# Optimization experiments

Hardware: AMD Instinct MI355X
Metric: run time of the kernel (lower is better)

The kernel has to match this reference:

```python
import jax, jax.numpy as jnp
import numpy as np

N_QUBITS = 8
N_LAYERS = 3
BATCH = 8192


def setup_inputs() -> dict:
    key = jax.random.key(0)
    k0, k1, k2, k3 = jax.random.split(key, 4)
    return {
        "x": jax.random.normal(k0, (BATCH, N_QUBITS), jnp.float32),
        "quantum_weights": jax.random.normal(k1, (N_LAYERS, N_QUBITS, 2), jnp.float32) * 0.1,
        "W1": jax.random.normal(k2, (N_QUBITS, 64), jnp.float32) / np.float32(np.sqrt(N_QUBITS)),
        "b1": jnp.zeros((64,), jnp.float32),
        "W2": jax.random.normal(k3, (64, 256), jnp.float32) / np.float32(np.sqrt(64)),
        "b2": jnp.zeros((256,), jnp.float32),
    }


def _ry(theta):
    # RY(t) = [[cos t/2, -sin t/2], [sin t/2, cos t/2]]; theta: [] or [B]
    c = jnp.cos(theta * 0.5)
    s = jnp.sin(theta * 0.5)
    U = jnp.stack([jnp.stack([c, -s], axis=-1), jnp.stack([s, c], axis=-1)], axis=-2)
    return U.astype(jnp.complex64)


def _rz(theta):
    # RZ(t) = diag(e^{-it/2}, e^{it/2})
    em = jnp.exp(-0.5j * theta.astype(jnp.complex64))
    ep = jnp.exp(0.5j * theta.astype(jnp.complex64))
    z = jnp.zeros_like(em)
    return jnp.stack([jnp.stack([em, z], axis=-1), jnp.stack([z, ep], axis=-1)], axis=-2)


def _apply_1q(state, U, q):
    # state: [B, 2,2,...,2]; qubit q lives on axis q+1. U: [2,2] (shared) or [B,2,2].
    s = jnp.moveaxis(state, q + 1, -1)
    if U.ndim == 3:
        s = jnp.einsum('b...i,bji->b...j', s, U)
    else:
        s = jnp.einsum('b...i,ji->b...j', s, U)
    return jnp.moveaxis(s, -1, q + 1)


def _cnot(state, c, t):
    # flip target bit on the control=1 slice
    s = jnp.moveaxis(state, (c + 1, t + 1), (1, 2))
    s = jnp.stack([s[:, 0], s[:, 1, ::-1]], axis=1)
    return jnp.moveaxis(s, (1, 2), (c + 1, t + 1))


def _quantum_forward(x, qw):
    B = x.shape[0]
    xmin = x.min(axis=1, keepdims=True)
    xmax = x.max(axis=1, keepdims=True)
    xn = (x - xmin) / (xmax - xmin + 1e-8)
    # |0...0> state, shape [B, 2]*n
    state = jnp.zeros((B,) + (2,) * N_QUBITS, jnp.complex64)
    state = state.at[(slice(None),) + (0,) * N_QUBITS].set(1.0)
    # feature encoding: RY(x_norm * pi), per-sample angles
    for q in range(N_QUBITS):
        state = _apply_1q(state, _ry(xn[:, q] * jnp.pi), q)
    # variational layers
    for layer in range(N_LAYERS):
        for q in range(N_QUBITS):
            state = _apply_1q(state, _ry(qw[layer, q, 0]), q)
            state = _apply_1q(state, _rz(qw[layer, q, 1]), q)
        for q in range(N_QUBITS):
            state = _cnot(state, q, (q + 1) % N_QUBITS)
    probs = jnp.real(state * jnp.conj(state))  # [B, 2]*n, float32
    z = []
    for q in range(N_QUBITS):
        p = probs.sum(axis=tuple(a for a in range(1, N_QUBITS + 1) if a != q + 1))
        z.append(p[:, 0] - p[:, 1])  # <Z_q>
    return jnp.stack(z, axis=1)  # [B, n_qubits]


def reference(x, quantum_weights, W1, b1, W2, b2):
    z = _quantum_forward(x, quantum_weights).astype(jnp.float32)
    h = jax.nn.relu(z @ W1 + b1)
    return h @ W2 + b2
```

## Files before the change

kernel.cpp:

```cpp
#include <hip/hip_runtime.h>

#define NQ 8
#define NLAYERS 3

typedef unsigned int uint2ev __attribute__((ext_vector_type(2)));
typedef float f2 __attribute__((ext_vector_type(2)));

template<int MASK>
__device__ __forceinline__ float xorlane(float v, int r) {
    if constexpr (MASK == 1) {
        return __int_as_float(__builtin_amdgcn_mov_dpp(__float_as_int(v), 0xB1, 0xF, 0xF, false));
    } else if constexpr (MASK == 2) {
        return __int_as_float(__builtin_amdgcn_mov_dpp(__float_as_int(v), 0x4E, 0xF, 0xF, false));
    } else if constexpr (MASK == 4) {
        float a = __int_as_float(__builtin_amdgcn_update_dpp(0, __float_as_int(v), 0x114, 0xF, 0xF, false));
        float b = __int_as_float(__builtin_amdgcn_update_dpp(0, __float_as_int(v), 0x104, 0xF, 0xF, false));
        return (r & 4) ? a : b;
    } else if constexpr (MASK == 8) {
        return __int_as_float(__builtin_amdgcn_mov_dpp(__float_as_int(v), 0x128, 0xF, 0xF, false));
    }
}

template<int MASK>
__device__ __forceinline__ f2 xorlane2(f2 v, int r) {
    f2 o;
    o.x = xorlane<MASK>(v.x, r);
    o.y = xorlane<MASK>(v.y, r);
    return o;
}

template<int CTRL>
__device__ __forceinline__ float dpp_add_stage(float v) {
    int moved = __builtin_amdgcn_update_dpp(0, __float_as_int(v), CTRL, 0xF, 0xF, false);
    return v + __int_as_float(moved);
}
__device__ __forceinline__ float rowsum15(float v) {
    v = dpp_add_stage<0x111>(v);
    v = dpp_add_stage<0x112>(v);
    v = dpp_add_stage<0x114>(v);
    v = dpp_add_stage<0x118>(v);
    return v;
}

__device__ __forceinline__ f2 cmul(f2 a, f2 b) {
    f2 r;
    r.x = a.x * b.x - a.y * b.y;
    r.y = a.x * b.y + a.y * b.x;
    return r;
}

__device__ __forceinline__ f2 splat(float c) { f2 v; v.x = c; v.y = c; return v; }

__device__ __forceinline__ f2 sel2(bool hi, f2 a, f2 b) {
    f2 o;
    o.x = hi ? a.x : b.x;
    o.y = hi ? a.y : b.y;
    return o;
}

template<int Q>
__device__ __forceinline__ void ry16(float c, float s, f2 A[16], int r) {
    f2 vc = splat(c), vs = splat(s);
    if constexpr (Q < 4) {
        constexpr int M = 1 << Q;
#pragma unroll
        for (int j = 0; j < 16; ++j) if (!(j & M)) {
            f2 a0 = A[j], a1 = A[j | M];
            A[j]     = vc * a0 - vs * a1;
            A[j | M] = vs * a0 + vc * a1;
        }
    } else {
        constexpr int LM = 1 << (Q - 4);
        f2 vsg = (r & LM) ? vs : (splat(0.f) - vs);
#pragma unroll
        for (int j = 0; j < 16; ++j) {
            f2 p = xorlane2<LM>(A[j], r);
            A[j] = vc * A[j] + vsg * p;
        }
    }
}

__device__ __forceinline__ void ring16(f2 A[16], int r) {
    f2 t;
    t = A[1]; A[1] = A[3]; A[3] = t;
    t = A[5]; A[5] = A[7]; A[7] = t;
    t = A[9]; A[9] = A[11]; A[11] = t;
    t = A[13]; A[13] = A[15]; A[15] = t;
    t = A[2]; A[2] = A[6]; A[6] = t;
    t = A[3]; A[3] = A[7]; A[7] = t;
    t = A[10]; A[10] = A[14]; A[14] = t;
    t = A[11]; A[11] = A[15]; A[15] = t;
    t = A[4]; A[4] = A[12]; A[12] = t;
    t = A[5]; A[5] = A[13]; A[13] = t;
    t = A[6]; A[6] = A[14]; A[14] = t;
    t = A[7]; A[7] = A[15]; A[15] = t;
#pragma unroll
    for (int j = 8; j < 16; ++j) A[j] = xorlane2<1>(A[j], r);
    {
        bool hi = (r & 1) != 0;
#pragma unroll
        for (int j = 0; j < 16; ++j) {
            f2 p = xorlane2<2>(A[j], r);
            A[j] = sel2(hi, p, A[j]);
        }
    }
    {
        bool hi = (r & 2) != 0;
#pragma unroll
        for (int j = 0; j < 16; ++j) {
            f2 p = xorlane2<4>(A[j], r);
            A[j] = sel2(hi, p, A[j]);
        }
    }
    {
        bool hi = (r & 4) != 0;
#pragma unroll
        for (int j = 0; j < 16; ++j) {
            f2 p = xorlane2<8>(A[j], r);
            A[j] = sel2(hi, p, A[j]);
        }
    }
    {
        bool hi = (r & 8) != 0;
#pragma unroll
        for (int j = 0; j < 16; j += 2) {
            f2 t0 = A[j], t1 = A[j + 1];
            A[j]     = sel2(hi, t1, t0);
            A[j + 1] = sel2(hi, t0, t1);
        }
    }
}

__global__ __launch_bounds__(256) void qfused(
    const float* __restrict__ x,
    const float* __restrict__ qw,
    const float* __restrict__ W1,
    const float* __restrict__ b1,
    const float* __restrict__ W2,
    const float* __restrict__ b2,
    float* __restrict__ out,
    int B)
{
    __shared__ float4 tab[NLAYERS * NQ];
    __shared__ float z_lds[16][8];
    __shared__ float h_lds[16][64];

    int tid = threadIdx.x;
    if (tid < NLAYERS * NQ) {
        float w0 = 0.5f * qw[tid * 2 + 0];
        float w1 = 0.5f * qw[tid * 2 + 1];
        if (tid < 8)
            tab[tid] = make_float4(w0, 0.f, __cosf(w1), __sinf(w1));
        else
            tab[tid] = make_float4(__cosf(w0), __sinf(w0), __cosf(w1), __sinf(w1));
    }
    __syncthreads();

    int lane = tid & 63;
    int wid  = tid >> 6;
    int g    = lane >> 4;
    int r    = lane & 15;
    int sl   = wid * 4 + g;
    int sbase = blockIdx.x * 16;
    int sample = sbase + sl;
    if (sample >= B) sample = B - 1;

    const float4* x4 = (const float4*)(x + sample * 8);
    float4 xa = x4[0], xb = x4[1];
    float xs[8] = {xa.x, xa.y, xa.z, xa.w, xb.x, xb.y, xb.z, xb.w};
    float xmin = xs[0], xmax = xs[0];
#pragma unroll
    for (int q = 1; q < 8; ++q) {
        xmin = fminf(xmin, xs[q]);
        xmax = fmaxf(xmax, xs[q]);
    }
    float inv_pi2 = 1.5707963267948966f / (xmax - xmin + 1e-8f);

    float cc[8], ss[8], cw[8], sw[8];
#pragma unroll
    for (int q = 0; q < 8; ++q) {
        float4 t0 = tab[q];
        float a = fmaf(xs[q] - xmin, inv_pi2, t0.x);
        __sincosf(a, &ss[q], &cc[q]);
        cw[q] = t0.z;
        sw[q] = t0.w;
    }

    int r0v = r & 1, r3v = (r >> 3) & 1;

    f2 X0[2], X1[2], X2[2], X3[2], X4[2];
#pragma unroll
    for (int k = 0; k < 2; ++k) {
        { int b = k ^ r3v; float rr = b ? ss[0] : cc[0];
          X0[k].x = rr * cw[0]; X0[k].y = (b ? rr : -rr) * sw[0]; }
        { int b = k ^ r3v; float rr = b ? ss[1] : cc[1];
          X1[k].x = rr * cw[1]; X1[k].y = (b ? rr : -rr) * sw[1]; }
        { int b = k;        float rr = b ? ss[2] : cc[2];
          X2[k].x = rr * cw[2]; X2[k].y = (b ? rr : -rr) * sw[2]; }
        { int b = k;        float rr = b ? ss[3] : cc[3];
          X3[k].x = rr * cw[3]; X3[k].y = (b ? rr : -rr) * sw[3]; }
        { int b = k ^ r0v;  float rr = b ? ss[4] : cc[4];
          X4[k].x = rr * cw[4]; X4[k].y = (b ? rr : -rr) * sw[4]; }
    }

    f2 pl;
    {
        int b5 = (r ^ (r >> 1)) & 1;
        int b6 = ((r >> 1) ^ (r >> 2)) & 1;
        int b7 = ((r >> 2) ^ (r >> 3)) & 1;
        f2 f5, f6, f7;
        float r5 = b5 ? ss[5] : cc[5];
        f5.x = r5 * cw[5]; f5.y = (b5 ? r5 : -r5) * sw[5];
        float r6 = b6 ? ss[6] : cc[6];
        f6.x = r6 * cw[6]; f6.y = (b6 ? r6 : -r6) * sw[6];
        float r7 = b7 ? ss[7] : cc[7];
        f7.x = r7 * cw[7]; f7.y = (b7 ? r7 : -r7) * sw[7];
        pl = cmul(cmul(f5, f6), f7);
    }

    f2 PP[2][2];
    {
        f2 t0 = cmul(pl, X0[0]);
        f2 t1 = cmul(pl, X0[1]);
        PP[0][0] = cmul(t0, X1[0]);
        PP[0][1] = cmul(t0, X1[1]);
        PP[1][0] = cmul(t1, X1[1]);
        PP[1][1] = cmul(t1, X1[0]);
    }
    f2 Q34[2][2];
    Q34[0][0] = cmul(X3[0], X4[0]);
    Q34[0][1] = cmul(X3[1], X4[1]);
    Q34[1][0] = cmul(X3[1], X4[0]);
    Q34[1][1] = cmul(X3[0], X4[1]);
    f2 R[2][2][2];
#pragma unroll
    for (int j1 = 0; j1 < 2; ++j1)
#pragma unroll
        for (int j2 = 0; j2 < 2; ++j2)
#pragma unroll
            for (int j3 = 0; j3 < 2; ++j3)
                R[j1][j2][j3] = cmul(X2[j1 ^ j2], Q34[j2][j3]);

    f2 A[16];
#pragma unroll
    for (int j3 = 0; j3 < 2; ++j3)
#pragma unroll
        for (int j2 = 0; j2 < 2; ++j2)
#pragma unroll
            for (int j1 = 0; j1 < 2; ++j1)
#pragma unroll
                for (int j0 = 0; j0 < 2; ++j0) {
                    int j = j0 + 2 * j1 + 4 * j2 + 8 * j3;
                    A[j] = cmul(PP[j0][j1], R[j1][j2][j3]);
                }

    {
        float4 t;
        t = tab[8];  ry16<0>(t.x, t.y, A, r);
        t = tab[9];  ry16<1>(t.x, t.y, A, r);
        t = tab[10]; ry16<2>(t.x, t.y, A, r);
        t = tab[11]; ry16<3>(t.x, t.y, A, r);
        t = tab[12]; ry16<4>(t.x, t.y, A, r);
        t = tab[13]; ry16<5>(t.x, t.y, A, r);
        t = tab[14]; ry16<6>(t.x, t.y, A, r);
        t = tab[15]; ry16<7>(t.x, t.y, A, r);
    }

    {
        f2 L;
        {
            float4 t4 = tab[12], t5 = tab[13], t6 = tab[14], t7 = tab[15];
            f2 d4, d5, d6, d7;
            d4.x = t4.z; d4.y = (r & 1) ? t4.w : -t4.w;
            d5.x = t5.z; d5.y = (r & 2) ? t5.w : -t5.w;
            d6.x = t6.z; d6.y = (r & 4) ? t6.w : -t6.w;
            d7.x = t7.z; d7.y = (r & 8) ? t7.w : -t7.w;
            L = cmul(cmul(d4, d5), cmul(d6, d7));
        }
        float4 t0q = tab[8], t1q = tab[9], t2q = tab[10], t3q = tab[11];
        f2 d0n, d0p, d1n, d1p, d2n, d2p, d3n, d3p;
        d0n.x = t0q.z; d0n.y = -t0q.w;  d0p.x = t0q.z; d0p.y = t0q.w;
        d1n.x = t1q.z; d1n.y = -t1q.w;  d1p.x = t1q.z; d1p.y = t1q.w;
        d2n.x = t2q.z; d2n.y = -t2q.w;  d2p.x = t2q.z; d2p.y = t2q.w;
        d3n.x = t3q.z; d3n.y = -t3q.w;  d3p.x = t3q.z; d3p.y = t3q.w;

        f2 t01[4];
        {
            f2 l0 = cmul(L, d0n), l1 = cmul(L, d0p);
            t01[0] = cmul(l0, d1n);
            t01[1] = cmul(l1, d1n);
            t01[2] = cmul(l0, d1p);
            t01[3] = cmul(l1, d1p);
        }
        f2 m23[4];
        m23[0] = cmul(d2n, d3n);
        m23[1] = cmul(d2p, d3n);
        m23[2] = cmul(d2n, d3p);
        m23[3] = cmul(d2p, d3p);

#pragma unroll
        for (int j = 0; j < 16; ++j) {
            f2 D = cmul(t01[j & 3], m23[j >> 2]);
            A[j] = cmul(A[j], D);
        }
    }

    ring16(A, r);

    {
        float4 t;
        t = tab[16]; ry16<0>(t.x, t.y, A, r);
        t = tab[17]; ry16<1>(t.x, t.y, A, r);
        t = tab[18]; ry16<2>(t.x, t.y, A, r);
        t = tab[19]; ry16<3>(t.x, t.y, A, r);
        t = tab[20]; ry16<4>(t.x, t.y, A, r);
        t = tab[21]; ry16<5>(t.x, t.y, A, r);
        t = tab[22]; ry16<6>(t.x, t.y, A, r);
        t = tab[23]; ry16<7>(t.x, t.y, A, r);
    }

    float P[16];
#pragma unroll
    for (int j = 0; j < 16; ++j) P[j] = A[j].x * A[j].x + A[j].y * A[j].y;

    float Sp[8], Dp[8];
#pragma unroll
    for (int k = 0; k < 8; ++k) {
        Sp[k] = P[2 * k] + P[2 * k + 1];
        Dp[k] = P[2 * k] - P[2 * k + 1];
    }
    float U0 = ((Sp[0] - Sp[1]) - (Sp[2] - Sp[3])) - ((Sp[4] - Sp[5]) - (Sp[6] - Sp[7]));
    float U3 = ((Dp[0] - Dp[1]) - (Dp[2] - Dp[3])) - ((Dp[4] - Dp[5]) - (Dp[6] - Dp[7]));
    float U1 = (Dp[0] - Dp[1]) + (Dp[2] - Dp[3]) + (Dp[4] - Dp[5]) + (Dp[6] - Dp[7]);
    float U2 = ((Dp[0] - Dp[1]) - (Dp[2] - Dp[3])) + ((Dp[4] - Dp[5]) - (Dp[6] - Dp[7]));

    int p1 = r & 1;
    int p2 = (r ^ (r >> 1)) & 1;
    int p3 = (r ^ (r >> 1) ^ (r >> 2)) & 1;
    int p4 = (r ^ (r >> 1) ^ (r >> 2) ^ (r >> 3)) & 1;

    float z0 = rowsum15(p4 ? -U0 : U0);
    float z1 = rowsum15(U1);
    float z2 = rowsum15(U2);
    float z3 = rowsum15(U3);
    float z4 = rowsum15(p1 ? -U3 : U3);
    float z5 = rowsum15(p2 ? -U3 : U3);
    float z6 = rowsum15(p3 ? -U3 : U3);
    float z7 = rowsum15(p4 ? -U3 : U3);

    if (r == 15) {
        *(float4*)&z_lds[sl][0] = make_float4(z0, z1, z2, z3);
        *(float4*)&z_lds[sl][4] = make_float4(z4, z5, z6, z7);
    }
    __syncthreads();

    {
        int s_l = tid >> 4;
        int i_l = (tid & 15) * 4;
        float4 za = *(const float4*)&z_lds[s_l][0];
        float4 zb = *(const float4*)&z_lds[s_l][4];
        float zq[8] = {za.x, za.y, za.z, za.w, zb.x, zb.y, zb.z, zb.w};
        float4 acc = *(const float4*)(b1 + i_l);
#pragma unroll
        for (int q = 0; q < 8; ++q) {
            float4 w = *(const float4*)(W1 + q * 64 + i_l);
            acc.x += zq[q] * w.x; acc.y += zq[q] * w.y;
            acc.z += zq[q] * w.z; acc.w += zq[q] * w.w;
        }
        acc.x = fmaxf(acc.x, 0.f); acc.y = fmaxf(acc.y, 0.f);
        acc.z = fmaxf(acc.z, 0.f); acc.w = fmaxf(acc.w, 0.f);
        *(float4*)&h_lds[s_l][i_l] = acc;
    }
    __syncthreads();

    int sg = tid >> 6;
    int c4 = (tid & 63) * 4;
    float4 bb = *(const float4*)(b2 + c4);
    float4 a0 = bb, a1 = bb, a2 = bb, a3 = bb;
    const int sO = sg * 4;

#pragma unroll 2
    for (int i4 = 0; i4 < 16; ++i4) {
        const float* wrow = W2 + i4 * 4 * 256 + c4;
        float4 w0 = *(const float4*)(wrow);
        float4 w1 = *(const float4*)(wrow + 256);
        float4 w2 = *(const float4*)(wrow + 512);
        float4 w3 = *(const float4*)(wrow + 768);
        float4 h0 = *(const float4*)&h_lds[sO + 0][i4 * 4];
        float4 h1 = *(const float4*)&h_lds[sO + 1][i4 * 4];
        float4 h2 = *(const float4*)&h_lds[sO + 2][i4 * 4];
        float4 h3 = *(const float4*)&h_lds[sO + 3][i4 * 4];

        a0.x += h0.x*w0.x + h0.y*w1.x + h0.z*w2.x + h0.w*w3.x;
        a0.y += h0.x*w0.y + h0.y*w1.y + h0.z*w2.y + h0.w*w3.y;
        a0.z += h0.x*w0.z + h0.y*w1.z + h0.z*w2.z + h0.w*w3.z;
        a0.w += h0.x*w0.w + h0.y*w1.w + h0.z*w2.w + h0.w*w3.w;

        a1.x += h1.x*w0.x + h1.y*w1.x + h1.z*w2.x + h1.w*w3.x;
        a1.y += h1.x*w0.y + h1.y*w1.y + h1.z*w2.y + h1.w*w3.y;
        a1.z += h1.x*w0.z + h1.y*w1.z + h1.z*w2.z + h1.w*w3.z;
        a1.w += h1.x*w0.w + h1.y*w1.w + h1.z*w2.w + h1.w*w3.w;

        a2.x += h2.x*w0.x + h2.y*w1.x + h2.z*w2.x + h2.w*w3.x;
        a2.y += h2.x*w0.y + h2.y*w1.y + h2.z*w2.y + h2.w*w3.y;
        a2.z += h2.x*w0.z + h2.y*w1.z + h2.z*w2.z + h2.w*w3.z;
        a2.w += h2.x*w0.w + h2.y*w1.w + h2.z*w2.w + h2.w*w3.w;

        a3.x += h3.x*w0.x + h3.y*w1.x + h3.z*w2.x + h3.w*w3.x;
        a3.y += h3.x*w0.y + h3.y*w1.y + h3.z*w2.y + h3.w*w3.y;
        a3.z += h3.x*w0.z + h3.y*w1.z + h3.z*w2.z + h3.w*w3.z;
        a3.w += h3.x*w0.w + h3.y*w1.w + h3.z*w2.w + h3.w*w3.w;
    }

    int srow = sbase + sO;
    if (srow + 0 < B) *(float4*)(out + (srow + 0) * 256 + c4) = a0;
    if (srow + 1 < B) *(float4*)(out + (srow + 1) * 256 + c4) = a1;
    if (srow + 2 < B) *(float4*)(out + (srow + 2) * 256 + c4) = a2;
    if (srow + 3 < B) *(float4*)(out + (srow + 3) * 256 + c4) = a3;
}

extern "C" void kernel_launch(void* const* d_in, const int* in_sizes, int n_in,
                              void* d_out, int out_size, void* d_ws, size_t ws_size,
                              hipStream_t stream) {
    const float* x  = (const float*)d_in[0];
    const float* qw = (const float*)d_in[1];
    const float* W1 = (const float*)d_in[2];
    const float* b1 = (const float*)d_in[3];
    const float* W2 = (const float*)d_in[4];
    const float* b2 = (const float*)d_in[5];
    float* out = (float*)d_out;

    int B = in_sizes[0] / NQ;

    qfused<<<(B + 15) / 16, 256, 0, stream>>>(x, qw, W1, b1, W2, b2, out, B);
}
```

Before: 20.10 us.

## Halve block size, use ds_swizzle for xor-4 lane exchange, hoist table loads

Changes the block from 256 to 128 threads, each handling 8 samples instead of 16, and doubles the grid so more blocks can spread across CUs. The xor-by-4 lane exchange now uses a single ds_swizzle instead of two DPP moves and a select. All per-layer rotation table entries are loaded from LDS into registers once at the start rather than reloaded at each use. The swizzle goes through the LDS crossbar and may add latency, and the hoisted loads raise register pressure.

```diff
diff --git a/kernel.cpp b/kernel.cpp
--- a/kernel.cpp
+++ b/kernel.cpp
@@ -13,9 +13,7 @@
     } else if constexpr (MASK == 2) {
         return __int_as_float(__builtin_amdgcn_mov_dpp(__float_as_int(v), 0x4E, 0xF, 0xF, false));
     } else if constexpr (MASK == 4) {
-        float a = __int_as_float(__builtin_amdgcn_update_dpp(0, __float_as_int(v), 0x114, 0xF, 0xF, false));
-        float b = __int_as_float(__builtin_amdgcn_update_dpp(0, __float_as_int(v), 0x104, 0xF, 0xF, false));
-        return (r & 4) ? a : b;
+        return __int_as_float(__builtin_amdgcn_ds_swizzle(__float_as_int(v), 0x101F));
     } else if constexpr (MASK == 8) {
         return __int_as_float(__builtin_amdgcn_mov_dpp(__float_as_int(v), 0x128, 0xF, 0xF, false));
     }
@@ -131,7 +129,7 @@
     }
 }
 
-__global__ __launch_bounds__(256) void qfused(
+__global__ __launch_bounds__(128) void qfused(
     const float* __restrict__ x,
     const float* __restrict__ qw,
     const float* __restrict__ W1,
@@ -142,8 +140,8 @@
     int B)
 {
     __shared__ float4 tab[NLAYERS * NQ];
-    __shared__ float z_lds[16][8];
-    __shared__ float h_lds[16][64];
+    __shared__ float z_lds[8][8];
+    __shared__ float h_lds[8][64];
 
     int tid = threadIdx.x;
     if (tid < NLAYERS * NQ) {
@@ -161,9 +159,14 @@
     int g    = lane >> 4;
     int r    = lane & 15;
     int sl   = wid * 4 + g;
-    int sbase = blockIdx.x * 16;
+    int sbase = blockIdx.x * 8;
     int sample = sbase + sl;
     if (sample >= B) sample = B - 1;
+
+    float4 T8 = tab[8],  T9 = tab[9],  T10 = tab[10], T11 = tab[11];
+    float4 T12 = tab[12], T13 = tab[13], T14 = tab[14], T15 = tab[15];
+    float4 T16 = tab[16], T17 = tab[17], T18 = tab[18], T19 = tab[19];
+    float4 T20 = tab[20], T21 = tab[21], T22 = tab[22], T23 = tab[23];
 
     const float4* x4 = (const float4*)(x + sample * 8);
     float4 xa = x4[0], xb = x4[1];
@@ -254,35 +257,30 @@
                     A[j] = cmul(PP[j0][j1], R[j1][j2][j3]);
                 }
 
-    {
-        float4 t;
-        t = tab[8];  ry16<0>(t.x, t.y, A, r);
-        t = tab[9];  ry16<1>(t.x, t.y, A, r);
-        t = tab[10]; ry16<2>(t.x, t.y, A, r);
-        t = tab[11]; ry16<3>(t.x, t.y, A, r);
-        t = tab[12]; ry16<4>(t.x, t.y, A, r);
-        t = tab[13]; ry16<5>(t.x, t.y, A, r);
-        t = tab[14]; ry16<6>(t.x, t.y, A, r);
-        t = tab[15]; ry16<7>(t.x, t.y, A, r);
-    }
+    ry16<0>(T8.x,  T8.y,  A, r);
+    ry16<1>(T9.x,  T9.y,  A, r);
+    ry16<2>(T10.x, T10.y, A, r);
+    ry16<3>(T11.x, T11.y, A, r);
+    ry16<4>(T12.x, T12.y, A, r);
+    ry16<5>(T13.x, T13.y, A, r);
+    ry16<6>(T14.x, T14.y, A, r);
+    ry16<7>(T15.x, T15.y, A, r);
 
     {
         f2 L;
         {
-            float4 t4 = tab[12], t5 = tab[13], t6 = tab[14], t7 = tab[15];
             f2 d4, d5, d6, d7;
-            d4.x = t4.z; d4.y = (r & 1) ? t4.w : -t4.w;
-            d5.x = t5.z; d5.y = (r & 2) ? t5.w : -t5.w;
-            d6.x = t6.z; d6.y = (r & 4) ? t6.w : -t6.w;
-            d7.x = t7.z; d7.y = (r & 8) ? t7.w : -t7.w;
+            d4.x = T12.z; d4.y = (r & 1) ? T12.w : -T12.w;
+            d5.x = T13.z; d5.y = (r & 2) ? T13.w : -T13.w;
+            d6.x = T14.z; d6.y = (r & 4) ? T14.w : -T14.w;
+            d7.x = T15.z; d7.y = (r & 8) ? T15.w : -T15.w;
             L = cmul(cmul(d4, d5), cmul(d6, d7));
         }
-        float4 t0q = tab[8], t1q = tab[9], t2q = tab[10], t3q = tab[11];
         f2 d0n, d0p, d1n, d1p, d2n, d2p, d3n, d3p;
-        d0n.x = t0q.z; d0n.y = -t0q.w;  d0p.x = t0q.z; d0p.y = t0q.w;
-        d1n.x = t1q.z; d1n.y = -t1q.w;  d1p.x = t1q.z; d1p.y = t1q.w;
-        d2n.x = t2q.z; d2n.y = -t2q.w;  d2p.x = t2q.z; d2p.y = t2q.w;
-        d3n.x = t3q.z; d3n.y = -t3q.w;  d3p.x = t3q.z; d3p.y = t3q.w;
+        d0n.x = T8.z;  d0n.y = -T8.w;   d0p.x = T8.z;  d0p.y = T8.w;
+        d1n.x = T9.z;  d1n.y = -T9.w;   d1p.x = T9.z;  d1p.y = T9.w;
+        d2n.x = T10.z; d2n.y = -T10.w;  d2p.x = T10.z; d2p.y = T10.w;
+        d3n.x = T11.z; d3n.y = -T11.w;  d3p.x = T11.z; d3p.y = T11.w;
 
         f2 t01[4];
         {
@@ -307,17 +305,14 @@
 
     ring16(A, r);
 
-    {
-        float4 t;
-        t = tab[16]; ry16<0>(t.x, t.y, A, r);
-        t = tab[17]; ry16<1>(t.x, t.y, A, r);
-        t = tab[18]; ry16<2>(t.x, t.y, A, r);
-        t = tab[19]; ry16<3>(t.x, t.y, A, r);
-        t = tab[20]; ry16<4>(t.x, t.y, A, r);
-        t = tab[21]; ry16<5>(t.x, t.y, A, r);
-        t = tab[22]; ry16<6>(t.x, t.y, A, r);
-        t = tab[23]; ry16<7>(t.x, t.y, A, r);
-    }
+    ry16<0>(T16.x, T16.y, A, r);
+    ry16<1>(T17.x, T17.y, A, r);
+    ry16<2>(T18.x, T18.y, A, r);
+    ry16<3>(T19.x, T19.y, A, r);
+    ry16<4>(T20.x, T20.y, A, r);
+    ry16<5>(T21.x, T21.y, A, r);
+    ry16<6>(T22.x, T22.y, A, r);
+    ry16<7>(T23.x, T23.y, A, r);
 
     float P[16];
 #pragma unroll
@@ -432,5 +427,5 @@
 
     int B = in_sizes[0] / NQ;
 
-    qfused<<<(B + 15) / 16, 256, 0, stream>>>(x, qw, W1, b1, W2, b2, out, B);
-}
+    qfused<<<(B + 7) / 8, 128, 0, stream>>>(x, qw, W1, b1, W2, b2, out, B);
+}
```

Result: no change. 20.18 us (+0.4%).
